# Performance work log

Hardware: AMD Instinct MI355X
Metric: run time of the kernel (lower is better)

The kernel has to match this reference:

```python
import jax, jax.numpy as jnp
import numpy as np

EMBED_DIM = 1024
BATCH, SEQ = 4, 2048


def setup_inputs() -> dict:
    key = jax.random.key(0)
    k1, k2 = jax.random.split(key)
    hidden_states = jax.random.normal(k1, (BATCH, SEQ, EMBED_DIM), dtype=jnp.float32)
    # fused QKV projection weight (Linear(embed_dim, 3*embed_dim, bias=False)),
    # stored as [E, 3E] so y = x @ W
    W_qkv = jax.random.normal(k2, (EMBED_DIM, 3 * EMBED_DIM), dtype=jnp.float32) * (1.0 / np.sqrt(EMBED_DIM))
    return {"hidden_states": hidden_states, "W_qkv": W_qkv}


def reference(hidden_states, W_qkv):
    E = hidden_states.shape[-1]
    scale = 1.0 / np.sqrt(E)
    qkv = jnp.einsum('bse,ef->bsf', hidden_states, W_qkv)  # [B,S,3E]
    q, k, v = jnp.split(qkv, 3, axis=-1)                   # each [B,S,E]
    # scores = q @ (k^T * scale); softmax over keys
    scores = jnp.einsum('bqe,bke->bqk', q, k) * scale      # [B,S,S]
    w = jax.nn.softmax(scores, axis=-1)
    return jnp.einsum('bqk,bke->bqe', w, v)                # [B,S,E]
```

## Files before the change

### kernel.cpp

```cpp
#include <hip/hip_runtime.h>

typedef __attribute__((ext_vector_type(8))) short short8;
typedef __attribute__((ext_vector_type(8))) unsigned short ushort8;
typedef __attribute__((ext_vector_type(4))) float f32x4;

__device__ __forceinline__ float bf2f(unsigned short u) {
  union { unsigned int u; float f; } c; c.u = ((unsigned int)u) << 16; return c.f;
}
__device__ __forceinline__ unsigned short f2bf(float f) {
  union { float f; unsigned int u; } c; c.f = f;
  unsigned int x = c.u;
  return (unsigned short)((x + 0x7FFFu + ((x >> 16) & 1u)) >> 16);
}

#define GLD_LDS16(g, l)                                                        \
  __builtin_amdgcn_global_load_lds(                                            \
      (const __attribute__((address_space(1))) void*)(g),                      \
      (__attribute__((address_space(3))) void*)(l), 16, 0, 0)

__device__ __forceinline__ void bar() {
  asm volatile("" ::: "memory");
  __builtin_amdgcn_s_barrier();
  asm volatile("" ::: "memory");
}

__device__ __forceinline__ void xcd_swizzle(int& bx, int& by, int& b) {
  const int gx = gridDim.x, gy = gridDim.y;
  const int nwg = gx * gy * (int)gridDim.z;
  const int id = blockIdx.x + gx * (blockIdx.y + gy * blockIdx.z);
  const int cpx = nwg >> 3;
  const int sid = (id & 7) * cpx + (id >> 3);
  by = sid % gy;
  const int tmp = sid / gy;
  bx = tmp % gx;
  b = tmp / gx;
}

__global__ __launch_bounds__(256) void prep_kernel(
    const float* __restrict__ X, unsigned short* __restrict__ Xb,
    const float* __restrict__ W, unsigned short* __restrict__ Wt,
    float* __restrict__ Lrow) {
  const int t = threadIdx.x;
  if (blockIdx.x < 4096) {
    long i = ((long)blockIdx.x * 256 + t) * 8;
    float4 a = *(const float4*)(X + i);
    float4 b = *(const float4*)(X + i + 4);
    ushort8 o;
    o[0] = f2bf(a.x); o[1] = f2bf(a.y); o[2] = f2bf(a.z); o[3] = f2bf(a.w);
    o[4] = f2bf(b.x); o[5] = f2bf(b.y); o[6] = f2bf(b.z); o[7] = f2bf(b.w);
    *(ushort8*)(Xb + i) = o;
  } else if (blockIdx.x < 4864) {
    const int bid = blockIdx.x - 4096;
    const int f0 = (bid % 48) * 64;
    const int e0 = (bid / 48) * 64;
    __shared__ unsigned short tile[64][65];
    const int cg = (t & 15) * 4;
    const int r = t >> 4;
#pragma unroll
    for (int i = 0; i < 4; ++i) {
      int e = r + i * 16;
      float4 v = *(const float4*)(W + (long)(e0 + e) * 3072 + f0 + cg);
      tile[e][cg + 0] = f2bf(v.x);
      tile[e][cg + 1] = f2bf(v.y);
      tile[e][cg + 2] = f2bf(v.z);
      tile[e][cg + 3] = f2bf(v.w);
    }
    __syncthreads();
#pragma unroll
    for (int i = 0; i < 4; ++i) {
      int f = (t >> 4) + i * 16;
      int e = (t & 15) * 4;
      ushort4 o;
      o.x = tile[e + 0][f];
      o.y = tile[e + 1][f];
      o.z = tile[e + 2][f];
      o.w = tile[e + 3][f];
      *(ushort4*)(Wt + (long)(f0 + f) * 1024 + e0 + e) = o;
    }
  } else {
    float4 z = {0.f, 0.f, 0.f, 0.f};
#pragma unroll
    for (int j = 0; j < 8; ++j) *(float4*)(Lrow + (j * 256 + t) * 4) = z;
  }
}

template <int MODE>
__device__ __forceinline__ void gemm256_body(
    const unsigned short* __restrict__ A, const unsigned short* __restrict__ B,
    void* __restrict__ Cv, int K, int lda, int ldb, int ldc,
    long sA, long sB, long sC, float alpha, float* __restrict__ Lrow,
    unsigned short* __restrict__ Vt) {
  __shared__ __align__(16) unsigned short smem[65536];

  const int t = threadIdx.x;
  const int lane = t & 63;
  const int wave = t >> 6;
  const int quad = lane >> 4;
  const int mrow = lane & 15;
  const int wm = wave >> 2;
  const int wn = wave & 3;

  int bx, by, b;
  xcd_swizzle(bx, by, b);
  const int rowA0 = by * 256;
  const int rowB0 = bx * 256;
  const unsigned short* Ab = A + (long)b * sA;
  const unsigned short* Bb = B + (long)b * sB;

  const int srow = lane >> 3;
  const int scol = ((lane & 7) ^ srow) * 8;

  const unsigned short* gA[4];
  const unsigned short* gB[4];
#pragma unroll
  for (int j = 0; j < 4; ++j) {
    gA[j] = Ab + (long)(rowA0 + j * 64 + wave * 8 + srow) * lda + scol;
    gB[j] = Bb + (long)(rowB0 + j * 64 + wave * 8 + srow) * ldb + scol;
  }
  const int dst = wave * 512;

  f32x4 acc[8][4];
#pragma unroll
  for (int i = 0; i < 8; ++i)
#pragma unroll
    for (int j = 0; j < 4; ++j) {
      f32x4 z = {0.f, 0.f, 0.f, 0.f};
      acc[i][j] = z;
    }

  const int NT = K >> 6;

  {
#pragma unroll
    for (int j = 0; j < 4; ++j) GLD_LDS16(gA[j], smem + j * 4096 + dst);
#pragma unroll
    for (int j = 0; j < 4; ++j)
      GLD_LDS16(gB[j], smem + 16384 + j * 4096 + dst);
    if (NT > 1) {
      GLD_LDS16(gB[0] + 64, smem + 32768 + 16384 + 0 * 4096 + dst);
      GLD_LDS16(gB[1] + 64, smem + 32768 + 16384 + 1 * 4096 + dst);
      asm volatile("s_waitcnt vmcnt(2)" ::: "memory");
    } else {
      asm volatile("s_waitcnt vmcnt(0)" ::: "memory");
    }
    bar();
  }

  const int m7 = mrow & 7;
  const int aslot0 = (quad ^ m7) * 8;

  for (int T = 0; T < NT; ++T) {
    const int boff = (T & 1) << 15;
    const int noff = boff ^ 32768;
    const unsigned short* As = smem + boff;
    const unsigned short* Bs = smem + boff + 16384;
    const int kt1 = (T + 1) << 6;
    const int kt2 = (T + 2) << 6;
    short8 af[4], bf[4];

#pragma unroll
    for (int i = 0; i < 4; ++i)
      af[i] = *(const short8*)(As + (wm * 128 + i * 16 + mrow) * 64 + aslot0);
#pragma unroll
    for (int j = 0; j < 4; ++j)
      bf[j] = *(const short8*)(Bs + (wn * 64 + j * 16 + mrow) * 64 + aslot0);
    if (T + 1 < NT) {
      GLD_LDS16(gB[2] + kt1, smem + noff + 16384 + 2 * 4096 + dst);
      GLD_LDS16(gB[3] + kt1, smem + noff + 16384 + 3 * 4096 + dst);
      GLD_LDS16(gA[0] + kt1, smem + noff + 0 * 4096 + dst);
      GLD_LDS16(gA[2] + kt1, smem + noff + 2 * 4096 + dst);
    }
    bar();
    __builtin_amdgcn_sched_barrier(0);
    __builtin_amdgcn_s_setprio(1);
#pragma unroll
    for (int i = 0; i < 4; ++i)
#pragma unroll
      for (int j = 0; j < 4; ++j)
        acc[i][j] = __builtin_amdgcn_mfma_f32_16x16x32_bf16(af[i], bf[j],
                                                            acc[i][j], 0, 0, 0);
    __builtin_amdgcn_s_setprio(0);
    __builtin_amdgcn_sched_barrier(0);
    bar();

#pragma unroll
    for (int i = 0; i < 4; ++i)
      af[i] =
          *(const short8*)(As + (wm * 128 + 64 + i * 16 + mrow) * 64 + aslot0);
    if (T + 1 < NT) {
      GLD_LDS16(gA[1] + kt1, smem + noff + 1 * 4096 + dst);
      GLD_LDS16(gA[3] + kt1, smem + noff + 3 * 4096 + dst);
    }
    bar();
    __builtin_amdgcn_sched_barrier(0);
    __builtin_amdgcn_s_setprio(1);
#pragma unroll
    for (int i = 0; i < 4; ++i)
#pragma unroll
      for (int j = 0; j < 4; ++j)
        acc[4 + i][j] = __builtin_amdgcn_mfma_f32_16x16x32_bf16(
            af[i], bf[j], acc[4 + i][j], 0, 0, 0);
    __builtin_amdgcn_s_setprio(0);
    __builtin_amdgcn_sched_barrier(0);
    bar();

#pragma unroll
    for (int i = 0; i < 4; ++i)
      af[i] = *(const short8*)(As + (wm * 128 + i * 16 + mrow) * 64 +
                               (aslot0 ^ 32));
#pragma unroll
    for (int j = 0; j < 4; ++j)
      bf[j] = *(const short8*)(Bs + (wn * 64 + j * 16 + mrow) * 64 +
                               (aslot0 ^ 32));
    bar();
    __builtin_amdgcn_sched_barrier(0);
    __builtin_amdgcn_s_setprio(1);
#pragma unroll
    for (int i = 0; i < 4; ++i)
#pragma unroll
      for (int j = 0; j < 4; ++j)
        acc[i][j] = __builtin_amdgcn_mfma_f32_16x16x32_bf16(af[i], bf[j],
                                                            acc[i][j], 0, 0, 0);
    __builtin_amdgcn_s_setprio(0);
    __builtin_amdgcn_sched_barrier(0);
    bar();

#pragma unroll
    for (int i = 0; i < 4; ++i)
      af[i] = *(const short8*)(As + (wm * 128 + 64 + i * 16 + mrow) * 64 +
                               (aslot0 ^ 32));
    if (T + 2 < NT) {
      GLD_LDS16(gB[0] + kt2, smem + boff + 16384 + 0 * 4096 + dst);
      GLD_LDS16(gB[1] + kt2, smem + boff + 16384 + 1 * 4096 + dst);
    }
    bar();
    __builtin_amdgcn_sched_barrier(0);
    __builtin_amdgcn_s_setprio(1);
#pragma unroll
    for (int i = 0; i < 4; ++i)
#pragma unroll
      for (int j = 0; j < 4; ++j)
        acc[4 + i][j] = __builtin_amdgcn_mfma_f32_16x16x32_bf16(
            af[i], bf[j], acc[4 + i][j], 0, 0, 0);
    __builtin_amdgcn_s_setprio(0);
    __builtin_amdgcn_sched_barrier(0);
    if (T + 2 < NT) {
      asm volatile("s_waitcnt vmcnt(2)" ::: "memory");
    } else {
      asm volatile("s_waitcnt vmcnt(0)" ::: "memory");
    }
    bar();
  }

  const long cb = (long)b * sC;

  if constexpr (MODE == 0) {
    if (bx < 8) {
      unsigned short* C = (unsigned short*)Cv;
#pragma unroll
      for (int m = 0; m < 8; ++m) {
        int row = rowA0 + wm * 128 + m * 16 + quad * 4;
#pragma unroll
        for (int j = 0; j < 4; ++j) {
          int col = rowB0 + wn * 64 + j * 16 + mrow;
#pragma unroll
          for (int r = 0; r < 4; ++r)
            C[(long)(row + r) * ldc + col] = f2bf(acc[m][j][r]);
        }
      }
    } else {
#pragma unroll
      for (int m = 0; m < 8; ++m) {
        int s4 = wm * 128 + m * 16 + quad * 4;
#pragma unroll
        for (int j = 0; j < 4; ++j) {
          int e = wn * 64 + j * 16 + mrow;
          int swz = ((e & 7) << 4) ^ (((e >> 3) & 3) << 3);
          ushort4 pk;
          pk.x = f2bf(acc[m][j][0]);
          pk.y = f2bf(acc[m][j][1]);
          pk.z = f2bf(acc[m][j][2]);
          pk.w = f2bf(acc[m][j][3]);
          *(ushort4*)(smem + e * 256 + (s4 ^ swz)) = pk;
        }
      }
      __syncthreads();
      const int batch = by >> 3;
      const int s_base = (by & 7) * 256;
      const int e_base = (bx - 8) * 256;
      unsigned short* VtB = Vt + (long)batch * 1024 * 2048;
      const int er = t >> 5;
      const int s = (t & 31) * 8;
#pragma unroll
      for (int rnd = 0; rnd < 16; ++rnd) {
        int e = rnd * 16 + er;
        int swz = ((e & 7) << 4) ^ (((e >> 3) & 3) << 3);
        ushort8 v = *(const ushort8*)(smem + e * 256 + (s ^ swz));
        *(ushort8*)(VtB + (long)(e_base + e) * 2048 + s_base + s) = v;
      }
    }
  } else {
    unsigned short* C = (unsigned short*)Cv;
    float p[8][4];
#pragma unroll
    for (int m = 0; m < 8; ++m)
#pragma unroll
      for (int r = 0; r < 4; ++r) p[m][r] = 0.f;
#pragma unroll
    for (int m = 0; m < 8; ++m) {
      int row = rowA0 + wm * 128 + m * 16 + quad * 4;
#pragma unroll
      for (int j = 0; j < 4; ++j) {
        int col = rowB0 + wn * 64 + j * 16 + mrow;
#pragma unroll
        for (int r = 0; r < 4; ++r) {
          float e = __expf(acc[m][j][r] * alpha);
          C[cb + (long)(row + r) * ldc + col] = f2bf(e);
          p[m][r] += e;
        }
      }
    }
#pragma unroll
    for (int off = 1; off < 16; off <<= 1)
#pragma unroll
      for (int m = 0; m < 8; ++m)
#pragma unroll
        for (int r = 0; r < 4; ++r)
          p[m][r] += __shfl_xor(p[m][r], off, 64);
    if (mrow == 0) {
#pragma unroll
      for (int m = 0; m < 8; ++m) {
        int row = rowA0 + wm * 128 + m * 16 + quad * 4;
#pragma unroll
        for (int r = 0; r < 4; ++r)
          atomicAdd(&Lrow[b * 2048 + row + r], p[m][r]);
      }
    }
  }
}

template <int MODE>
__device__ __forceinline__ void gemm_body(
    const unsigned short* __restrict__ A, const unsigned short* __restrict__ B,
    void* __restrict__ Cv, int K, int lda, int ldb, int ldc,
    long sA, long sB, long sC, float alpha, float* __restrict__ Lrow,
    unsigned short* __restrict__ Vt) {
  constexpr int BM = 128, BN = 128, BK = 64;
  __shared__ __align__(16) unsigned short smem[BM * BK + BN * BK];
  unsigned short* As = smem;
  unsigned short* Bs = smem + BM * BK;

  const int t = threadIdx.x;
  const int lane = t & 63;
  const int wave = t >> 6;
  const int quad = lane >> 4;
  const int mrow = lane & 15;
  const int wm = wave >> 1, wn = wave & 1;

  int bx, by, b;
  xcd_swizzle(bx, by, b);
  const int rowA0 = by * BM;
  const int rowB0 = bx * BN;
  const unsigned short* Ab = A + (long)b * sA;
  const unsigned short* Bb = B + (long)b * sB;

  f32x4 acc[4][4];
#pragma unroll
  for (int i = 0; i < 4; ++i)
#pragma unroll
    for (int j = 0; j < 4; ++j) {
      f32x4 z = {0.f, 0.f, 0.f, 0.f};
      acc[i][j] = z;
    }

  const int rbase = wave * 32 + (lane >> 3);
  const int c2 = lane & 7;

  for (int kt = 0; kt < K; kt += BK) {
#pragma unroll
    for (int j = 0; j < 4; ++j) {
      int r = rbase + j * 8;
      int c = c2 ^ (r & 7);
      GLD_LDS16(Ab + (long)(rowA0 + r) * lda + kt + c * 8, As + (wave * 4 + j) * 512);
      GLD_LDS16(Bb + (long)(rowB0 + r) * ldb + kt + c * 8, Bs + (wave * 4 + j) * 512);
    }
    __syncthreads();
#pragma unroll
    for (int ks = 0; ks < 2; ++ks) {
      short8 af[4], bfr[4];
#pragma unroll
      for (int i = 0; i < 4; ++i) {
        int rA = wm * 64 + i * 16 + mrow;
        int cc = ks * 4 + quad;
        af[i] = *(const short8*)(As + (rA * 8 + (cc ^ (rA & 7))) * 8);
        int rB = wn * 64 + i * 16 + mrow;
        bfr[i] = *(const short8*)(Bs + (rB * 8 + (cc ^ (rB & 7))) * 8);
      }
#pragma unroll
      for (int mt = 0; mt < 4; ++mt)
#pragma unroll
        for (int nt = 0; nt < 4; ++nt)
          acc[mt][nt] = __builtin_amdgcn_mfma_f32_16x16x32_bf16(
              af[mt], bfr[nt], acc[mt][nt], 0, 0, 0);
    }
    __syncthreads();
  }

  const int m_base = rowA0 + wm * 64;
  const int n_base = rowB0 + wn * 64;
  const long cb = (long)b * sC;

#pragma unroll
  for (int mt = 0; mt < 4; ++mt)
#pragma unroll
    for (int i = 0; i < 4; ++i) {
      int row = m_base + mt * 16 + quad * 4 + i;
      float inv = 1.0f / Lrow[b * 2048 + row];
#pragma unroll
      for (int nt = 0; nt < 4; ++nt) {
        int col = n_base + nt * 16 + mrow;
        ((float*)Cv)[cb + (long)row * ldc + col] = acc[mt][nt][i] * inv;
      }
    }
}

__global__ __launch_bounds__(512, 2) void qkv_gemm_kernel(
    const unsigned short* __restrict__ A, const unsigned short* __restrict__ B,
    void* __restrict__ Cv, int K, int lda, int ldb, int ldc,
    long sA, long sB, long sC, float alpha, float* __restrict__ Lrow,
    unsigned short* __restrict__ Vt) {
  gemm256_body<0>(A, B, Cv, K, lda, ldb, ldc, sA, sB, sC, alpha, Lrow, Vt);
}
__global__ __launch_bounds__(512, 2) void score_gemm_kernel(
    const unsigned short* __restrict__ A, const unsigned short* __restrict__ B,
    void* __restrict__ Cv, int K, int lda, int ldb, int ldc,
    long sA, long sB, long sC, float alpha, float* __restrict__ Lrow,
    unsigned short* __restrict__ Vt) {
  gemm256_body<1>(A, B, Cv, K, lda, ldb, ldc, sA, sB, sC, alpha, Lrow, Vt);
}
__global__ __launch_bounds__(256, 2) void out_gemm_kernel(
    const unsigned short* __restrict__ A, const unsigned short* __restrict__ B,
    void* __restrict__ Cv, int K, int lda, int ldb, int ldc,
    long sA, long sB, long sC, float alpha, float* __restrict__ Lrow,
    unsigned short* __restrict__ Vt) {
  gemm_body<2>(A, B, Cv, K, lda, ldb, ldc, sA, sB, sC, alpha, Lrow, Vt);
}

extern "C" void kernel_launch(void* const* d_in, const int* in_sizes, int n_in,
                              void* d_out, int out_size, void* d_ws, size_t ws_size,
                              hipStream_t stream) {
  const float* X = (const float*)d_in[0];
  const float* W = (const float*)d_in[1];
  float* out = (float*)d_out;

  char* ws = (char*)d_ws;
  unsigned short* Xb  = (unsigned short*)(ws);
  unsigned short* Wtb = (unsigned short*)(ws + 16777216);
  unsigned short* QK  = (unsigned short*)(ws + 23068672);
  unsigned short* Vt  = (unsigned short*)(ws + 56623104);
  unsigned short* Sb  = (unsigned short*)(ws + 73400320);
  float* Lrow         = (float*)(ws + 106954752);

  prep_kernel<<<4865, 256, 0, stream>>>(X, Xb, W, Wtb, Lrow);

  qkv_gemm_kernel<<<dim3(12, 32, 1), 512, 0, stream>>>(
      Xb, Wtb, QK, 1024, 1024, 1024, 2048, 0L, 0L, 0L, 1.0f, nullptr, Vt);

  score_gemm_kernel<<<dim3(8, 8, 4), 512, 0, stream>>>(
      QK, QK + 1024, Sb, 1024, 2048, 2048, 2048,
      (long)2048 * 2048, (long)2048 * 2048, (long)2048 * 2048, 0.03125f, Lrow, nullptr);

  out_gemm_kernel<<<dim3(8, 16, 4), 256, 0, stream>>>(
      Sb, Vt, out, 2048, 2048, 2048, 1024,
      (long)2048 * 2048, (long)1024 * 2048, (long)2048 * 1024, 1.0f, Lrow, nullptr);
}
```

Measured before the change: 237.6 us.

## Software-pipeline LDS fragment loads across MFMA phases and drop XCD swizzle

Restructures the 256x256 GEMM main loop so LDS fragment reads for the next phase (and the next k-tile) are issued before the current MFMA block. Partial lgkmcnt waits let those reads overlap with compute, and two barriers per k-tile are removed. The global prefetch schedule is simplified to load the whole next tile within one iteration. The XCD-aware block swizzle is also removed in favour of plain blockIdx mapping, which may change L2 locality across chiplets. Extra fragment registers (aN/bN) raise VGPR pressure, and the hand-written waitcnt counts must match the compiler's instruction order.

```diff
diff --git a/kernel.cpp b/kernel.cpp
--- a/kernel.cpp
+++ b/kernel.cpp
@@ -22,18 +22,6 @@
   asm volatile("" ::: "memory");
   __builtin_amdgcn_s_barrier();
   asm volatile("" ::: "memory");
-}
-
-__device__ __forceinline__ void xcd_swizzle(int& bx, int& by, int& b) {
-  const int gx = gridDim.x, gy = gridDim.y;
-  const int nwg = gx * gy * (int)gridDim.z;
-  const int id = blockIdx.x + gx * (blockIdx.y + gy * blockIdx.z);
-  const int cpx = nwg >> 3;
-  const int sid = (id & 7) * cpx + (id >> 3);
-  by = sid % gy;
-  const int tmp = sid / gy;
-  bx = tmp % gx;
-  b = tmp / gx;
 }
 
 __global__ __launch_bounds__(256) void prep_kernel(
@@ -100,8 +88,7 @@
   const int wm = wave >> 2;
   const int wn = wave & 3;
 
-  int bx, by, b;
-  xcd_swizzle(bx, by, b);
+  const int bx = blockIdx.x, by = blockIdx.y, b = blockIdx.z;
   const int rowA0 = by * 256;
   const int rowB0 = bx * 256;
   const unsigned short* Ab = A + (long)b * sA;
@@ -130,68 +117,74 @@
 
   const int NT = K >> 6;
 
+  const int m7 = mrow & 7;
+  const int aslot0 = (quad ^ m7) * 8;
+  const int arow0 = (wm * 128 + mrow) * 64;
+  const int brow0 = (wn * 64 + mrow) * 64;
+
+  short8 aC[4], aN[4], bC[4], bN[4];
+
   {
 #pragma unroll
     for (int j = 0; j < 4; ++j) GLD_LDS16(gA[j], smem + j * 4096 + dst);
 #pragma unroll
     for (int j = 0; j < 4; ++j)
       GLD_LDS16(gB[j], smem + 16384 + j * 4096 + dst);
-    if (NT > 1) {
-      GLD_LDS16(gB[0] + 64, smem + 32768 + 16384 + 0 * 4096 + dst);
-      GLD_LDS16(gB[1] + 64, smem + 32768 + 16384 + 1 * 4096 + dst);
-      asm volatile("s_waitcnt vmcnt(2)" ::: "memory");
-    } else {
-      asm volatile("s_waitcnt vmcnt(0)" ::: "memory");
-    }
+    asm volatile("s_waitcnt vmcnt(0)" ::: "memory");
     bar();
-  }
-
-  const int m7 = mrow & 7;
-  const int aslot0 = (quad ^ m7) * 8;
+#pragma unroll
+    for (int i = 0; i < 4; ++i)
+      aC[i] = *(const short8*)(smem + arow0 + i * 1024 + aslot0);
+#pragma unroll
+    for (int j = 0; j < 4; ++j)
+      bC[j] = *(const short8*)(smem + 16384 + brow0 + j * 1024 + aslot0);
+  }
 
   for (int T = 0; T < NT; ++T) {
     const int boff = (T & 1) << 15;
     const int noff = boff ^ 32768;
     const unsigned short* As = smem + boff;
     const unsigned short* Bs = smem + boff + 16384;
+    const unsigned short* Asn = smem + noff;
+    const unsigned short* Bsn = smem + noff + 16384;
     const int kt1 = (T + 1) << 6;
-    const int kt2 = (T + 2) << 6;
-    short8 af[4], bf[4];
-
-#pragma unroll
-    for (int i = 0; i < 4; ++i)
-      af[i] = *(const short8*)(As + (wm * 128 + i * 16 + mrow) * 64 + aslot0);
-#pragma unroll
-    for (int j = 0; j < 4; ++j)
-      bf[j] = *(const short8*)(Bs + (wn * 64 + j * 16 + mrow) * 64 + aslot0);
-    if (T + 1 < NT) {
+    const bool more = (T + 1) < NT;
+
+#pragma unroll
+    for (int i = 0; i < 4; ++i)
+      aN[i] = *(const short8*)(As + arow0 + 4096 + i * 1024 + aslot0);
+    if (more) {
+      GLD_LDS16(gA[0] + kt1, smem + noff + 0 * 4096 + dst);
+      GLD_LDS16(gA[2] + kt1, smem + noff + 2 * 4096 + dst);
+      GLD_LDS16(gB[0] + kt1, smem + noff + 16384 + 0 * 4096 + dst);
+      GLD_LDS16(gB[1] + kt1, smem + noff + 16384 + 1 * 4096 + dst);
       GLD_LDS16(gB[2] + kt1, smem + noff + 16384 + 2 * 4096 + dst);
       GLD_LDS16(gB[3] + kt1, smem + noff + 16384 + 3 * 4096 + dst);
-      GLD_LDS16(gA[0] + kt1, smem + noff + 0 * 4096 + dst);
-      GLD_LDS16(gA[2] + kt1, smem + noff + 2 * 4096 + dst);
     }
     bar();
+    asm volatile("s_waitcnt lgkmcnt(4)" ::: "memory");
     __builtin_amdgcn_sched_barrier(0);
     __builtin_amdgcn_s_setprio(1);
 #pragma unroll
     for (int i = 0; i < 4; ++i)
 #pragma unroll
       for (int j = 0; j < 4; ++j)
-        acc[i][j] = __builtin_amdgcn_mfma_f32_16x16x32_bf16(af[i], bf[j],
+        acc[i][j] = __builtin_amdgcn_mfma_f32_16x16x32_bf16(aC[i], bC[j],
                                                             acc[i][j], 0, 0, 0);
     __builtin_amdgcn_s_setprio(0);
-    __builtin_amdgcn_sched_barrier(0);
-    bar();
-
-#pragma unroll
-    for (int i = 0; i < 4; ++i)
-      af[i] =
-          *(const short8*)(As + (wm * 128 + 64 + i * 16 + mrow) * 64 + aslot0);
-    if (T + 1 < NT) {
+
+#pragma unroll
+    for (int i = 0; i < 4; ++i)
+      aC[i] = *(const short8*)(As + arow0 + i * 1024 + (aslot0 ^ 32));
+#pragma unroll
+    for (int j = 0; j < 4; ++j)
+      bN[j] = *(const short8*)(Bs + brow0 + j * 1024 + (aslot0 ^ 32));
+    if (more) {
       GLD_LDS16(gA[1] + kt1, smem + noff + 1 * 4096 + dst);
       GLD_LDS16(gA[3] + kt1, smem + noff + 3 * 4096 + dst);
     }
     bar();
+    asm volatile("s_waitcnt lgkmcnt(8)" ::: "memory");
     __builtin_amdgcn_sched_barrier(0);
     __builtin_amdgcn_s_setprio(1);
 #pragma unroll
@@ -199,41 +192,40 @@
 #pragma unroll
       for (int j = 0; j < 4; ++j)
         acc[4 + i][j] = __builtin_amdgcn_mfma_f32_16x16x32_bf16(
-            af[i], bf[j], acc[4 + i][j], 0, 0, 0);
+            aN[i], bC[j], acc[4 + i][j], 0, 0, 0);
     __builtin_amdgcn_s_setprio(0);
-    __builtin_amdgcn_sched_barrier(0);
+
+#pragma unroll
+    for (int i = 0; i < 4; ++i)
+      aN[i] = *(const short8*)(As + arow0 + 4096 + i * 1024 + (aslot0 ^ 32));
+    if (more) asm volatile("s_waitcnt vmcnt(2)" ::: "memory");
     bar();
-
-#pragma unroll
-    for (int i = 0; i < 4; ++i)
-      af[i] = *(const short8*)(As + (wm * 128 + i * 16 + mrow) * 64 +
-                               (aslot0 ^ 32));
-#pragma unroll
-    for (int j = 0; j < 4; ++j)
-      bf[j] = *(const short8*)(Bs + (wn * 64 + j * 16 + mrow) * 64 +
-                               (aslot0 ^ 32));
-    bar();
+    asm volatile("s_waitcnt lgkmcnt(4)" ::: "memory");
     __builtin_amdgcn_sched_barrier(0);
     __builtin_amdgcn_s_setprio(1);
 #pragma unroll
     for (int i = 0; i < 4; ++i)
 #pragma unroll
       for (int j = 0; j < 4; ++j)
-        acc[i][j] = __builtin_amdgcn_mfma_f32_16x16x32_bf16(af[i], bf[j],
+        acc[i][j] = __builtin_amdgcn_mfma_f32_16x16x32_bf16(aC[i], bN[j],
                                                             acc[i][j], 0, 0, 0);
     __builtin_amdgcn_s_setprio(0);
-    __builtin_amdgcn_sched_barrier(0);
+
+    if (more) {
+#pragma unroll
+      for (int i = 0; i < 4; ++i)
+        aC[i] = *(const short8*)(Asn + arow0 + i * 1024 + aslot0);
+#pragma unroll
+      for (int j = 0; j < 4; ++j)
+        bC[j] = *(const short8*)(Bsn + brow0 + j * 1024 + aslot0);
+      asm volatile("s_waitcnt vmcnt(0)" ::: "memory");
+    }
     bar();
-
-#pragma unroll
-    for (int i = 0; i < 4; ++i)
-      af[i] = *(const short8*)(As + (wm * 128 + 64 + i * 16 + mrow) * 64 +
-                               (aslot0 ^ 32));
-    if (T + 2 < NT) {
-      GLD_LDS16(gB[0] + kt2, smem + boff + 16384 + 0 * 4096 + dst);
-      GLD_LDS16(gB[1] + kt2, smem + boff + 16384 + 1 * 4096 + dst);
-    }
-    bar();
+    if (more) {
+      asm volatile("s_waitcnt lgkmcnt(8)" ::: "memory");
+    } else {
+      asm volatile("s_waitcnt lgkmcnt(0)" ::: "memory");
+    }
     __builtin_amdgcn_sched_barrier(0);
     __builtin_amdgcn_s_setprio(1);
 #pragma unroll
@@ -241,15 +233,8 @@
 #pragma unroll
       for (int j = 0; j < 4; ++j)
         acc[4 + i][j] = __builtin_amdgcn_mfma_f32_16x16x32_bf16(
-            af[i], bf[j], acc[4 + i][j], 0, 0, 0);
+            aN[i], bN[j], acc[4 + i][j], 0, 0, 0);
     __builtin_amdgcn_s_setprio(0);
-    __builtin_amdgcn_sched_barrier(0);
-    if (T + 2 < NT) {
-      asm volatile("s_waitcnt vmcnt(2)" ::: "memory");
-    } else {
-      asm volatile("s_waitcnt vmcnt(0)" ::: "memory");
-    }
-    bar();
   }
 
   const long cb = (long)b * sC;
@@ -269,6 +254,7 @@
         }
       }
     } else {
+      bar();
 #pragma unroll
       for (int m = 0; m < 8; ++m) {
         int s4 = wm * 128 + m * 16 + quad * 4;
@@ -357,10 +343,10 @@
   const int mrow = lane & 15;
   const int wm = wave >> 1, wn = wave & 1;
 
-  int bx, by, b;
-  xcd_swizzle(bx, by, b);
+  const int bx = blockIdx.x, by = blockIdx.y;
   const int rowA0 = by * BM;
   const int rowB0 = bx * BN;
+  const int b = blockIdx.z;
   const unsigned short* Ab = A + (long)b * sA;
   const unsigned short* Bb = B + (long)b * sB;
 
```

After: 239.1 us. About the same (+0.6%).
